# Optimization experiments

Measured on AMD Instinct MI355X. Metric: run time of the kernel, lower is better.

## Reference

```python
import jax, jax.numpy as jnp
import numpy as np

NEG = 1e9  # mask value added to already-selected positions (original uses -1e9)


def setup_inputs() -> dict:
    key = jax.random.key(0)
    ks = jax.random.split(key, 12)
    B, N, M = 8, 2048, 256
    s = 0.05  # keep gates/softmax in a sane range
    return dict(
        node_embedding=jax.random.normal(ks[0], (B, N, M), dtype=jnp.float32),
        z_g=jax.random.normal(ks[1], (B, M), dtype=jnp.float32) * s,
        decoder_init=jax.random.normal(ks[2], (M,), dtype=jnp.float32) * s,
        hidden0=jax.random.normal(ks[3], (M,), dtype=jnp.float32) * s,
        w_ih=jax.random.normal(ks[4], (4 * M, M), dtype=jnp.float32) * s,
        w_hh=jax.random.normal(ks[5], (4 * M, M), dtype=jnp.float32) * s,
        b_ih=jax.random.normal(ks[6], (4 * M,), dtype=jnp.float32) * s,
        b_hh=jax.random.normal(ks[7], (4 * M,), dtype=jnp.float32) * s,
        Wq=jax.random.normal(ks[8], (M, M), dtype=jnp.float32) * s,
        bq=jax.random.normal(ks[9], (M,), dtype=jnp.float32) * s,
        Wk=jax.random.normal(ks[10], (M, M), dtype=jnp.float32) * s,
        bk=jax.random.normal(ks[11], (M,), dtype=jnp.float32) * s,
    )


def reference(node_embedding, z_g, decoder_init, hidden0,
              w_ih, w_hh, b_ih, b_hh, Wq, bq, Wk, bk):
    # Returns the per-step masked softmax attention distributions [B, N, N]
    # (row t = distribution over boxes at decode step t; argmax of each row
    #  is the predicted order, and selected indices are masked out).
    N = node_embedding.shape[1]
    # LSTM input is the constant decoder_init every step -> precompute its proj.
    x_proj = decoder_init @ w_ih.T + b_ih  # [4M]

    def decode_one(z_g_b, node_emb_b):
        keys = node_emb_b @ Wk.T + bk  # [N, M] (self.key(node_embedding))

        def step(carry, _):
            h, c, used = carry
            # torch LSTMCell: gates ordered (i, f, g, o)
            gates = x_proj + h @ w_hh.T + b_hh  # [4M]
            i_g, f_g, g_g, o_g = jnp.split(gates, 4)
            i_g = jax.nn.sigmoid(i_g)
            f_g = jax.nn.sigmoid(f_g)
            g_g = jnp.tanh(g_g)
            o_g = jax.nn.sigmoid(o_g)
            c = f_g * c + i_g * g_g
            h = o_g * jnp.tanh(c)
            q = h @ Wq.T + bq                    # [M]
            scores = keys @ q                    # [N]
            scores = jnp.where(used, scores - NEG, scores)  # mask selected
            probs = jax.nn.softmax(scores)       # [N]
            idx = jnp.argmax(probs)              # top-1 pointer selection
            used = used.at[idx].set(True)
            return (h, c, used), probs

        init = (hidden0, z_g_b, jnp.zeros((N,), dtype=bool))
        _, probs = jax.lax.scan(step, init, None, length=N)
        return probs  # [N, N]

    return jax.vmap(decode_one)(z_g, node_embedding)  # [B, N, N]
```

## Files before the change

kernel.cpp:

```cpp
#include <hip/hip_runtime.h>
#include <cstdint>
#include <cstddef>

#define NB 8
#define NN 2048
#define MM 256

typedef unsigned long long u64;

__device__ __forceinline__ unsigned mapf(float f) {
  unsigned u = __float_as_uint(f + 0.f);
  return ((int)u >= 0) ? (u ^ 0x80000000u) : ~u;
}
__device__ __forceinline__ u64 shflx_u64(u64 v, int m) {
  unsigned lo = (unsigned)__shfl_xor((int)(unsigned)v, m);
  unsigned hi = (unsigned)__shfl_xor((int)(v >> 32), m);
  return ((u64)hi << 32) | lo;
}

__device__ __forceinline__ u64 load_sc0(const u64* p) {
  u64 v;
  asm volatile("global_load_dwordx2 %0, %1, off sc0\n\ts_waitcnt vmcnt(0)"
               : "=v"(v) : "v"(p) : "memory");
  return v;
}
__device__ __forceinline__ void store_plain(u64* p, u64 v) {
  asm volatile("global_store_dwordx2 %0, %1, off" :: "v"(p), "v"(v) : "memory");
}

__global__ __launch_bounds__(1024) void lstm_kernel(
    const float* __restrict__ z_g, const float* __restrict__ dec,
    const float* __restrict__ h0, const float* __restrict__ w_ih,
    const float* __restrict__ w_hh, const float* __restrict__ b_ih,
    const float* __restrict__ b_hh, const float* __restrict__ Wq,
    const float* __restrict__ bq, float* __restrict__ Qout,
    u64* __restrict__ Hfast, u64* __restrict__ Hslow)
{
  const int b = blockIdx.x;
  const int j = blockIdx.y;
  const int tid = threadIdx.x;
  const int w = tid >> 6;
  const int lane = tid & 63;
  const int q = w & 7;
  const int rg = w >> 3;
  const int lr = rg * 64 + lane;
  const int g = lr >> 5;
  const int mi = lr & 31;
  const int grow = g * 256 + 32 * j + mi;

  __shared__ __align__(16) float part[2][128 * 12];
  __shared__ __align__(16) float part2[2][32 * 36];

  float wreg[32];
  {
    const float* wr = w_hh + (size_t)grow * MM + 32 * q;
    #pragma unroll
    for (int i = 0; i < 8; ++i) {
      float4 v = *(const float4*)(wr + 4 * i);
      wreg[4 * i + 0] = v.x; wreg[4 * i + 1] = v.y;
      wreg[4 * i + 2] = v.z; wreg[4 * i + 3] = v.w;
    }
  }
  float wqa[8];
  {
    const float* wr = Wq + (size_t)(32 * j + mi) * MM + 32 * q + 8 * g;
    float4 w0 = *(const float4*)(wr);
    float4 w1 = *(const float4*)(wr + 4);
    wqa[0] = w0.x; wqa[1] = w0.y; wqa[2] = w0.z; wqa[3] = w0.w;
    wqa[4] = w1.x; wqa[5] = w1.y; wqa[6] = w1.z; wqa[7] = w1.w;
  }
  const float bqv = (w == 1 && lane < 32) ? bq[32 * j + lane] : 0.f;

  {
    float p = 0.f;
    const float* wr = w_ih + (size_t)grow * MM + 32 * q;
    #pragma unroll
    for (int i = 0; i < 8; ++i) {
      float4 wv = *(const float4*)(wr + 4 * i);
      float4 dv = *(const float4*)(dec + 32 * q + 4 * i);
      p += wv.x * dv.x + wv.y * dv.y + wv.z * dv.z + wv.w * dv.w;
    }
    part[0][lr * 12 + q] = p;
  }
  __syncthreads();

  float xbA = 0.f, xbB = 0.f, c_my = 0.f;
  if (w == 0) {
    #pragma unroll
    for (int rr = 0; rr < 2; ++rr) {
      const int lr2 = lane + rr * 64;
      const int g2 = lr2 >> 5, mi2 = lr2 & 31;
      const int grow2 = g2 * 256 + 32 * j + mi2;
      float4 p0 = *(const float4*)&part[0][lr2 * 12];
      float4 p1 = *(const float4*)&part[0][lr2 * 12 + 4];
      const float xb = p0.x + p0.y + p0.z + p0.w + p1.x + p1.y + p1.z + p1.w
                     + b_ih[grow2] + b_hh[grow2];
      if (rr == 0) xbA = xb; else xbB = xb;
    }
    if (lane < 32) c_my = z_g[b * MM + 32 * j + lane];
  }
  __syncthreads();

  u64* Hf = Hfast + (size_t)b * 512;
  u64* Hs = Hslow + (size_t)b * 512;
  const int hidx = 32 * q + (lane & 31);

  for (int t = 0; t <= NN; ++t) {
    int hvi;
    if (t == 0) {
      hvi = __float_as_int(h0[hidx]);
    } else {
      const int off = ((t & 1) << 8) + hidx;
      u64 v = load_sc0(Hf + off);
      bool slow = false;
      for (;;) {
        const bool ok = ((unsigned)(v >> 32) == (unsigned)t);
        if (__all((int)ok)) break;
        slow = !slow;
        if (!ok) {
          v = slow ? __hip_atomic_load(Hs + off, __ATOMIC_RELAXED,
                                       __HIP_MEMORY_SCOPE_AGENT)
                   : load_sc0(Hf + off);
        }
      }
      hvi = (int)(unsigned)v;
    }

    {
      float a0 = 0.f, a1 = 0.f, a2 = 0.f, a3 = 0.f;
      #pragma unroll
      for (int k = 0; k < 32; k += 4) {
        a0 = fmaf(__uint_as_float((unsigned)__builtin_amdgcn_readlane(hvi, k + 0)), wreg[k + 0], a0);
        a1 = fmaf(__uint_as_float((unsigned)__builtin_amdgcn_readlane(hvi, k + 1)), wreg[k + 1], a1);
        a2 = fmaf(__uint_as_float((unsigned)__builtin_amdgcn_readlane(hvi, k + 2)), wreg[k + 2], a2);
        a3 = fmaf(__uint_as_float((unsigned)__builtin_amdgcn_readlane(hvi, k + 3)), wreg[k + 3], a3);
      }
      part[t & 1][lr * 12 + q] = (a0 + a1) + (a2 + a3);
    }

    {
      float qa = 0.f;
      #pragma unroll
      for (int i = 0; i < 8; ++i) {
        const float hh = __uint_as_float((unsigned)__shfl(hvi, 8 * g + i));
        qa = fmaf(hh, wqa[i], qa);
      }
      if (t > 0) part2[t & 1][mi * 36 + q * 4 + g] = qa;
    }
    __syncthreads();

    if (w == 0 && t < NN) {
      const float* pp = &part[t & 1][0];
      float4 A0 = *(const float4*)(pp + lane * 12);
      float4 A1 = *(const float4*)(pp + lane * 12 + 4);
      float4 B0 = *(const float4*)(pp + (lane + 64) * 12);
      float4 B1 = *(const float4*)(pp + (lane + 64) * 12 + 4);
      const float vA = xbA + A0.x + A0.y + A0.z + A0.w + A1.x + A1.y + A1.z + A1.w;
      const float vB = xbB + B0.x + B0.y + B0.z + B0.w + B1.x + B1.y + B1.z + B1.w;
      const float s1 = 1.f / (1.f + __expf(-vA));
      const float e  = __expf(((lane < 32) ? -2.f : -1.f) * vB);
      const float s2 = (lane < 32) ? (2.f / (1.f + e) - 1.f)
                                   : (1.f / (1.f + e));
      const float fo1 = __shfl_xor(s1, 32);
      const float fo2 = __shfl_xor(s2, 32);
      if (lane < 32) {
        c_my = fo1 * c_my + s1 * s2;
        const float e2 = __expf(-2.f * c_my);
        const float hn = fo2 * (2.f / (1.f + e2) - 1.f);
        const u64 pk = ((u64)(unsigned)(t + 1) << 32) | (u64)__float_as_uint(hn);
        const int so = (((t + 1) & 1) << 8) + 32 * j + lane;
        store_plain(Hf + so, pk);
        __hip_atomic_store(Hs + so, pk, __ATOMIC_RELAXED,
                           __HIP_MEMORY_SCOPE_AGENT);
      }
    }

    if (w == 1 && t > 0 && lane < 32) {
      float s = 0.f;
      #pragma unroll
      for (int c = 0; c < 8; ++c) {
        float4 p = *(const float4*)&part2[t & 1][lane * 36 + 4 * c];
        s += p.x + p.y + p.z + p.w;
      }
      Qout[((size_t)b * NN + (t - 1)) * MM + 32 * j + lane] = s + bqv;
    }
  }
}

__global__ __launch_bounds__(256) void gemm128(
    const float* __restrict__ A, const float* __restrict__ B,
    float* __restrict__ C, const float* __restrict__ bias,
    int K, int Ncol, long sA, long sB, long sC)
{
  __shared__ __align__(16) float As[32][132];
  __shared__ __align__(16) float Bs[32][132];
  const int tid = threadIdx.x;
  const int tx = tid & 15;
  const int ty = tid >> 4;
  const int row0 = blockIdx.y * 128;
  const int col0 = blockIdx.x * 128;
  const float* Ab = A + (size_t)blockIdx.z * (size_t)sA;
  const float* Bb = B + (size_t)blockIdx.z * (size_t)sB;
  float* Cb = C + (size_t)blockIdx.z * (size_t)sC;

  float acc[8][8];
  #pragma unroll
  for (int i = 0; i < 8; ++i)
    #pragma unroll
    for (int jj = 0; jj < 8; ++jj) acc[i][jj] = 0.f;

  for (int k0 = 0; k0 < K; k0 += 32) {
    #pragma unroll
    for (int it = 0; it < 4; ++it) {
      const int idx = tid + it * 256;
      const int r = idx >> 3;
      const int c4 = (idx & 7) << 2;
      float4 va = *(const float4*)(Ab + (size_t)(row0 + r) * K + k0 + c4);
      float4 vb = *(const float4*)(Bb + (size_t)(col0 + r) * K + k0 + c4);
      As[c4 + 0][r] = va.x; As[c4 + 1][r] = va.y;
      As[c4 + 2][r] = va.z; As[c4 + 3][r] = va.w;
      Bs[c4 + 0][r] = vb.x; Bs[c4 + 1][r] = vb.y;
      Bs[c4 + 2][r] = vb.z; Bs[c4 + 3][r] = vb.w;
    }
    __syncthreads();
    #pragma unroll
    for (int kk = 0; kk < 32; ++kk) {
      float4 a0 = *(const float4*)&As[kk][ty * 4];
      float4 a1 = *(const float4*)&As[kk][64 + ty * 4];
      float4 b0 = *(const float4*)&Bs[kk][tx * 4];
      float4 b1 = *(const float4*)&Bs[kk][64 + tx * 4];
      const float av[8] = {a0.x, a0.y, a0.z, a0.w, a1.x, a1.y, a1.z, a1.w};
      const float bv[8] = {b0.x, b0.y, b0.z, b0.w, b1.x, b1.y, b1.z, b1.w};
      #pragma unroll
      for (int i = 0; i < 8; ++i)
        #pragma unroll
        for (int jj = 0; jj < 8; ++jj)
          acc[i][jj] = fmaf(av[i], bv[jj], acc[i][jj]);
    }
    __syncthreads();
  }

  #pragma unroll
  for (int i = 0; i < 8; ++i) {
    const int r = row0 + ((i < 4) ? (ty * 4 + i) : (64 + ty * 4 + i - 4));
    float* cp = Cb + (size_t)r * Ncol + col0;
    float4 o0, o1;
    float* o0p = &o0.x; float* o1p = &o1.x;
    #pragma unroll
    for (int jj = 0; jj < 4; ++jj) {
      float v0 = acc[i][jj], v1 = acc[i][jj + 4];
      if (bias) {
        v0 += bias[col0 + tx * 4 + jj];
        v1 += bias[col0 + 64 + tx * 4 + jj];
      }
      o0p[jj] = v0; o1p[jj] = v1;
    }
    *(float4*)(cp + tx * 4) = o0;
    *(float4*)(cp + 64 + tx * 4) = o1;
  }
}

__global__ __launch_bounds__(512) void select_block(
    const float* __restrict__ S, int* __restrict__ sel)
{
  const int b = blockIdx.x;
  const int tid = threadIdx.x;
  const int w = tid >> 6;
  const int lane = tid & 63;
  const float* Sb = S + (size_t)b * NN * NN + 4 * tid;
  int* selb = sel + b * NN;

  __shared__ u64 partial[2][8];

  for (int i = tid; i < NN; i += 512) selb[i] = 0x7fffffff;
  __syncthreads();

  unsigned mybits = 0;
  const unsigned base = 2047u - 4u * (unsigned)tid;

  auto stepf = [&](float4 v, int t) {
    u64 k0 = (mybits & 1u) ? 0 : (((u64)mapf(v.x) << 32) | (base - 0u));
    u64 k1 = (mybits & 2u) ? 0 : (((u64)mapf(v.y) << 32) | (base - 1u));
    u64 k2 = (mybits & 4u) ? 0 : (((u64)mapf(v.z) << 32) | (base - 2u));
    u64 k3 = (mybits & 8u) ? 0 : (((u64)mapf(v.w) << 32) | (base - 3u));
    u64 k = k0 > k1 ? k0 : k1;
    if (k2 > k) k = k2;
    if (k3 > k) k = k3;
    #pragma unroll
    for (int off = 1; off < 64; off <<= 1) {
      u64 o = shflx_u64(k, off);
      if (o > k) k = o;
    }
    if (lane == 0) partial[t & 1][w] = k;
    __syncthreads();
    u64 pk = partial[t & 1][lane & 7];
    #pragma unroll
    for (int off = 1; off < 8; off <<= 1) {
      u64 o = shflx_u64(pk, off);
      if (o > pk) pk = o;
    }
    const int idx = 2047 - (int)(pk & 0x7ff);
    if ((idx >> 2) == tid) mybits |= 1u << (idx & 3);
    if (tid == 0) selb[idx] = t;
  };

  float4 r0 = *(const float4*)(Sb + (size_t)0 * NN);
  float4 r1 = *(const float4*)(Sb + (size_t)1 * NN);
  float4 r2 = *(const float4*)(Sb + (size_t)2 * NN);
  float4 r3 = *(const float4*)(Sb + (size_t)3 * NN);
  for (int t = 0; t < NN; t += 4) {
    const size_t p4 = (size_t)((t + 4 < NN) ? t + 4 : NN - 1) * NN;
    const size_t p5 = (size_t)((t + 5 < NN) ? t + 5 : NN - 1) * NN;
    const size_t p6 = (size_t)((t + 6 < NN) ? t + 6 : NN - 1) * NN;
    const size_t p7 = (size_t)((t + 7 < NN) ? t + 7 : NN - 1) * NN;
    stepf(r0, t);     r0 = *(const float4*)(Sb + p4);
    stepf(r1, t + 1); r1 = *(const float4*)(Sb + p5);
    stepf(r2, t + 2); r2 = *(const float4*)(Sb + p6);
    stepf(r3, t + 3); r3 = *(const float4*)(Sb + p7);
  }
}

__global__ __launch_bounds__(256) void softmax_kernel(
    float* __restrict__ out, const int* __restrict__ sel)
{
  const int t = blockIdx.x;
  const int b = blockIdx.y;
  const int tid = threadIdx.x;
  float* row = out + ((size_t)b * NN + t) * NN;
  const int* selb = sel + b * NN;
  __shared__ float red[8];

  float v[8];
  int sl[8];
  #pragma unroll
  for (int u = 0; u < 2; ++u) {
    float4 f = *(const float4*)(row + u * 1024 + tid * 4);
    int4 s4 = *(const int4*)(selb + u * 1024 + tid * 4);
    v[u * 4 + 0] = f.x; v[u * 4 + 1] = f.y; v[u * 4 + 2] = f.z; v[u * 4 + 3] = f.w;
    sl[u * 4 + 0] = s4.x; sl[u * 4 + 1] = s4.y; sl[u * 4 + 2] = s4.z; sl[u * 4 + 3] = s4.w;
  }

  float mx = -3.0e38f;
  #pragma unroll
  for (int e = 0; e < 8; ++e)
    if (sl[e] >= t) mx = fmaxf(mx, v[e]);
  #pragma unroll
  for (int off = 1; off < 64; off <<= 1) mx = fmaxf(mx, __shfl_xor(mx, off));
  if ((tid & 63) == 0) red[tid >> 6] = mx;
  __syncthreads();
  mx = fmaxf(fmaxf(red[0], red[1]), fmaxf(red[2], red[3]));

  float e8[8];
  float sum = 0.f;
  #pragma unroll
  for (int e = 0; e < 8; ++e) {
    float ex = (sl[e] >= t) ? __expf(v[e] - mx) : 0.f;
    e8[e] = ex;
    sum += ex;
  }
  #pragma unroll
  for (int off = 1; off < 64; off <<= 1) sum += __shfl_xor(sum, off);
  if ((tid & 63) == 0) red[4 + (tid >> 6)] = sum;
  __syncthreads();
  sum = red[4] + red[5] + red[6] + red[7];
  const float inv = 1.f / sum;

  #pragma unroll
  for (int u = 0; u < 2; ++u) {
    float4 o;
    o.x = e8[u * 4 + 0] * inv; o.y = e8[u * 4 + 1] * inv;
    o.z = e8[u * 4 + 2] * inv; o.w = e8[u * 4 + 3] * inv;
    *(float4*)(row + u * 1024 + tid * 4) = o;
  }
}

extern "C" void kernel_launch(void* const* d_in, const int* in_sizes, int n_in,
                              void* d_out, int out_size, void* d_ws, size_t ws_size,
                              hipStream_t stream)
{
  (void)in_sizes; (void)n_in; (void)out_size; (void)ws_size;
  const float* emb  = (const float*)d_in[0];
  const float* z_g  = (const float*)d_in[1];
  const float* dec  = (const float*)d_in[2];
  const float* h0   = (const float*)d_in[3];
  const float* w_ih = (const float*)d_in[4];
  const float* w_hh = (const float*)d_in[5];
  const float* b_ih = (const float*)d_in[6];
  const float* b_hh = (const float*)d_in[7];
  const float* Wq   = (const float*)d_in[8];
  const float* bq   = (const float*)d_in[9];
  const float* Wk   = (const float*)d_in[10];
  const float* bk   = (const float*)d_in[11];
  float* out = (float*)d_out;
  float* ws  = (float*)d_ws;

  float* keys  = ws;
  float* Q     = ws + 4194304;
  u64*   Hfast = (u64*)(ws + 8388608);
  u64*   Hslow = (u64*)(ws + 8396800);
  int*   sel   = (int*)(ws + 8404992);

  lstm_kernel<<<dim3(NB, 8), 1024, 0, stream>>>(
      z_g, dec, h0, w_ih, w_hh, b_ih, b_hh, Wq, bq, Q, Hfast, Hslow);

  gemm128<<<dim3(MM / 128, (NB * NN) / 128, 1), 256, 0, stream>>>(
      emb, Wk, keys, bk, MM, MM, 0, 0, 0);

  gemm128<<<dim3(NN / 128, NN / 128, NB), 256, 0, stream>>>(
      Q, keys, out, nullptr, MM, NN,
      (long)NN * MM, (long)NN * MM, (long)NN * NN);

  select_block<<<NB, 512, 0, stream>>>(out, sel);

  softmax_kernel<<<dim3(NN, NB), 256, 0, stream>>>(out, sel);
}
```

Baseline: 5.101 ms.

## Mirror hidden state into LDS for critical warps and transpose partial-sum layout

Warps 0 and 1, which carry the per-step LSTM and query reductions, now poll a workgroup-shared mirror of h instead of global memory. Warps 8 and 9 fetch h from global and forward it into that mirror. The global polling loop now prefers the fast sc0 load and only occasionally falls back to the agent-scope atomic, decided once at step 1. The partial-sum LDS arrays are also transposed to a [q][row] layout with padding, so reductions read conflict-free scalars instead of float4s. Together these aim to cut global polling latency on the serial recurrence path, at the cost of an extra intra-block hop and a tighter reliance on workgroup-scope atomics being visible promptly.

```diff
diff --git a/kernel.cpp b/kernel.cpp
--- a/kernel.cpp
+++ b/kernel.cpp
@@ -48,8 +48,11 @@
   const int mi = lr & 31;
   const int grow = g * 256 + 32 * j + mi;
 
-  __shared__ __align__(16) float part[2][128 * 12];
-  __shared__ __align__(16) float part2[2][32 * 36];
+  __shared__ __align__(16) float part[2][8][128];
+  __shared__ __align__(16) float part2[2][32][33];
+  __shared__ __align__(16) u64 hmir[8][32];
+
+  if (tid < 256) ((u64*)hmir)[tid] = 0xAAAAAAAAAAAAAAAAull;
 
   float wreg[32];
   {
@@ -80,7 +83,7 @@
       float4 dv = *(const float4*)(dec + 32 * q + 4 * i);
       p += wv.x * dv.x + wv.y * dv.y + wv.z * dv.z + wv.w * dv.w;
     }
-    part[0][lr * 12 + q] = p;
+    part[0][q][lr] = p;
   }
   __syncthreads();
 
@@ -91,10 +94,9 @@
       const int lr2 = lane + rr * 64;
       const int g2 = lr2 >> 5, mi2 = lr2 & 31;
       const int grow2 = g2 * 256 + 32 * j + mi2;
-      float4 p0 = *(const float4*)&part[0][lr2 * 12];
-      float4 p1 = *(const float4*)&part[0][lr2 * 12 + 4];
-      const float xb = p0.x + p0.y + p0.z + p0.w + p1.x + p1.y + p1.z + p1.w
-                     + b_ih[grow2] + b_hh[grow2];
+      float xb = b_ih[grow2] + b_hh[grow2];
+      #pragma unroll
+      for (int qq = 0; qq < 8; ++qq) xb += part[0][qq][lr2];
       if (rr == 0) xbA = xb; else xbB = xb;
     }
     if (lane < 32) c_my = z_g[b * MM + 32 * j + lane];
@@ -104,25 +106,42 @@
   u64* Hf = Hfast + (size_t)b * 512;
   u64* Hs = Hslow + (size_t)b * 512;
   const int hidx = 32 * q + (lane & 31);
+  int fastok = 1;
 
   for (int t = 0; t <= NN; ++t) {
     int hvi;
     if (t == 0) {
       hvi = __float_as_int(h0[hidx]);
+    } else if (w < 2) {
+      u64 v;
+      for (;;) {
+        v = __hip_atomic_load(&hmir[q][lane & 31], __ATOMIC_RELAXED,
+                              __HIP_MEMORY_SCOPE_WORKGROUP);
+        if (__all((int)((unsigned)(v >> 32) == (unsigned)t))) break;
+      }
+      hvi = (int)(unsigned)v;
     } else {
       const int off = ((t & 1) << 8) + hidx;
       u64 v = load_sc0(Hf + off);
-      bool slow = false;
+      int tries = 0;
       for (;;) {
         const bool ok = ((unsigned)(v >> 32) == (unsigned)t);
         if (__all((int)ok)) break;
-        slow = !slow;
+        ++tries;
         if (!ok) {
-          v = slow ? __hip_atomic_load(Hs + off, __ATOMIC_RELAXED,
-                                       __HIP_MEMORY_SCOPE_AGENT)
-                   : load_sc0(Hf + off);
+          const bool useslow = fastok ? ((tries & 15) == 15) : true;
+          v = useslow ? __hip_atomic_load(Hs + off, __ATOMIC_RELAXED,
+                                          __HIP_MEMORY_SCOPE_AGENT)
+                      : load_sc0(Hf + off);
         }
       }
+      if (t == 1) {
+        const u64 pv = load_sc0(Hf + off);
+        fastok = __all((int)((unsigned)(pv >> 32) == 1u)) ? 1 : 0;
+      }
+      if ((w == 8 || w == 9) && lane < 32)
+        __hip_atomic_store(&hmir[q][lane], v, __ATOMIC_RELAXED,
+                           __HIP_MEMORY_SCOPE_WORKGROUP);
       hvi = (int)(unsigned)v;
     }
 
@@ -135,7 +154,7 @@
         a2 = fmaf(__uint_as_float((unsigned)__builtin_amdgcn_readlane(hvi, k + 2)), wreg[k + 2], a2);
         a3 = fmaf(__uint_as_float((unsigned)__builtin_amdgcn_readlane(hvi, k + 3)), wreg[k + 3], a3);
       }
-      part[t & 1][lr * 12 + q] = (a0 + a1) + (a2 + a3);
+      part[t & 1][q][lr] = (a0 + a1) + (a2 + a3);
     }
 
     {
@@ -145,18 +164,17 @@
         const float hh = __uint_as_float((unsigned)__shfl(hvi, 8 * g + i));
         qa = fmaf(hh, wqa[i], qa);
       }
-      if (t > 0) part2[t & 1][mi * 36 + q * 4 + g] = qa;
+      if (t > 0) part2[t & 1][g * 8 + q][mi] = qa;
     }
     __syncthreads();
 
     if (w == 0 && t < NN) {
-      const float* pp = &part[t & 1][0];
-      float4 A0 = *(const float4*)(pp + lane * 12);
-      float4 A1 = *(const float4*)(pp + lane * 12 + 4);
-      float4 B0 = *(const float4*)(pp + (lane + 64) * 12);
-      float4 B1 = *(const float4*)(pp + (lane + 64) * 12 + 4);
-      const float vA = xbA + A0.x + A0.y + A0.z + A0.w + A1.x + A1.y + A1.z + A1.w;
-      const float vB = xbB + B0.x + B0.y + B0.z + B0.w + B1.x + B1.y + B1.z + B1.w;
+      float vA = xbA, vB = xbB;
+      #pragma unroll
+      for (int qq = 0; qq < 8; ++qq) {
+        vA += part[t & 1][qq][lane];
+        vB += part[t & 1][qq][lane + 64];
+      }
       const float s1 = 1.f / (1.f + __expf(-vA));
       const float e  = __expf(((lane < 32) ? -2.f : -1.f) * vB);
       const float s2 = (lane < 32) ? (2.f / (1.f + e) - 1.f)
@@ -178,10 +196,7 @@
     if (w == 1 && t > 0 && lane < 32) {
       float s = 0.f;
       #pragma unroll
-      for (int c = 0; c < 8; ++c) {
-        float4 p = *(const float4*)&part2[t & 1][lane * 36 + 4 * c];
-        s += p.x + p.y + p.z + p.w;
-      }
+      for (int p = 0; p < 32; ++p) s += part2[t & 1][p][lane];
       Qout[((size_t)b * NN + (t - 1)) * MM + 32 * j + lane] = s + bqv;
     }
   }
```

Result: slower. 8.794 ms (+72.4%).
